# Kernel tuning notes

Measured on AMD Instinct MI355X. Metric: run time of the kernel, lower is better.

Reference implementation:

```python
import jax, jax.numpy as jnp
import numpy as np

N_EMBD = 1024  # C in forward; scale uses C**-0.5

def setup_inputs() -> dict:
    key = jax.random.key(0)
    k1, k2, k3, k4 = jax.random.split(key, 4)
    B, T, C, H = 4, 4096, N_EMBD, 64
    x = jax.random.normal(k1, (B, T, C), dtype=jnp.float32)
    # nn.Linear weights stored already-transposed as [in, out] for x @ W
    s = 1.0 / np.sqrt(C)
    Wq = jax.random.normal(k2, (C, H), dtype=jnp.float32) * s
    Wk = jax.random.normal(k3, (C, H), dtype=jnp.float32) * s
    Wv = jax.random.normal(k4, (C, H), dtype=jnp.float32) * s
    return {"x": x, "Wq": Wq, "Wk": Wk, "Wv": Wv}

def reference(x, Wq, Wk, Wv):
    B, T, C = x.shape
    q = jnp.einsum('btc,ch->bth', x, Wq)
    k = jnp.einsum('btc,ch->bth', x, Wk)
    v = jnp.einsum('btc,ch->bth', x, Wv)
    # scores scaled by C**-0.5 (note: original scales by embed dim, not head_size)
    wei = jnp.einsum('bth,bsh->bts', q, k) * (C ** -0.5)
    causal = jnp.tril(jnp.ones((T, T), dtype=bool))  # [T,T]
    wei = jnp.where(causal[None, :, :], wei, -jnp.inf)
    wei = jax.nn.softmax(wei, axis=-1)
    # dropout p=0.0 (eval-mode reference): identity
    out = jnp.einsum('bts,bsh->bth', wei, v)
    return out
```

## Files before the change

### kernel.cpp

```cpp
#include <hip/hip_runtime.h>

typedef __bf16 bf16x8 __attribute__((ext_vector_type(8)));
typedef float floatx16 __attribute__((ext_vector_type(16)));
typedef float floatx4 __attribute__((ext_vector_type(4)));

#define T_ 4096
#define STK 72
#define NSPB 144

#define WT_OFF 0u
#define Q_OFF  393216u
#define K_OFF  2490368u
#define V_OFF  4587520u
#define OP_OFF 6684672u
#define ML_OFF 25559040u

__device__ __forceinline__ unsigned short bf16bits(float f) {
  __bf16 h = (__bf16)f;
  return __builtin_bit_cast(unsigned short, h);
}

__global__ void wprep(const float* __restrict__ Wq, const float* __restrict__ Wk,
                      const float* __restrict__ Wv, __bf16* __restrict__ Wtg) {
  int idx = blockIdx.x * 256 + threadIdx.x;
  int mat = idx >> 16;
  int r = idx & 65535;
  int h = r & 63;
  int k = r >> 6;
  const float* W = (mat == 0) ? Wq : ((mat == 1) ? Wk : Wv);
  float v = W[k * 64 + h];
  if (mat == 0) v *= 0.03125f * 1.4426950408889634f;
  Wtg[(size_t)(mat * 64 + h) * 1024 + k] = (__bf16)v;
}

__global__ __launch_bounds__(256, 4) void proj(const float* __restrict__ x,
                                               const __bf16* __restrict__ Wtg,
                                               __bf16* __restrict__ Qp,
                                               __bf16* __restrict__ Kp,
                                               __bf16* __restrict__ Vp) {
  __shared__ __align__(16) unsigned short sm[(32 + 192) * STK];
  unsigned short* xt = sm;
  unsigned short* wt = sm + 32 * STK;
  const int tid = threadIdx.x;
  const int wave = tid >> 6, lane = tid & 63;
  const int wm = wave & 1, wn = wave >> 1;
  const int l15 = lane & 15, quad = lane >> 4;
  const size_t row0 = (size_t)blockIdx.x * 32;

  floatx4 acc[6];
#pragma unroll
  for (int t = 0; t < 6; t++)
#pragma unroll
    for (int i = 0; i < 4; i++) acc[t][i] = 0.0f;

  for (int kc = 0; kc < 16; ++kc) {
    __syncthreads();
    {
      int row = tid >> 3, seg = tid & 7;
      const float* src = x + (row0 + row) * 1024 + kc * 64 + seg * 8;
      float f[8];
      *(float4*)(f) = *(const float4*)(src);
      *(float4*)(f + 4) = *(const float4*)(src + 4);
      unsigned short hb[8];
#pragma unroll
      for (int i = 0; i < 8; i++) hb[i] = bf16bits(f[i]);
      *(uint4*)&xt[row * STK + seg * 8] = *(uint4*)(hb);
    }
#pragma unroll
    for (int i = 0; i < 6; i++) {
      int idx = tid + 256 * i;
      int r = idx >> 3, c = (idx & 7) * 8;
      *(uint4*)&wt[r * STK + c] = *(const uint4*)(Wtg + (size_t)r * 1024 + kc * 64 + c);
    }
    __syncthreads();
#pragma unroll
    for (int ks = 0; ks < 2; ++ks) {
      bf16x8 a = *(const bf16x8*)&xt[(wm * 16 + l15) * STK + ks * 32 + quad * 8];
#pragma unroll
      for (int ht = 0; ht < 6; ++ht) {
        bf16x8 b = *(const bf16x8*)&wt[(wn * 96 + ht * 16 + l15) * STK + ks * 32 + quad * 8];
        acc[ht] = __builtin_amdgcn_mfma_f32_16x16x32_bf16(a, b, acc[ht], 0, 0, 0);
      }
    }
  }
#pragma unroll
  for (int ht = 0; ht < 6; ++ht) {
    int g0 = wn * 96 + ht * 16;
    int mat = g0 >> 6, h0 = g0 & 63;
    __bf16* outp = (mat == 0) ? Qp : ((mat == 1) ? Kp : Vp);
#pragma unroll
    for (int r = 0; r < 4; r++) {
      size_t row = row0 + wm * 16 + quad * 4 + r;
      outp[row * 64 + h0 + l15] = (__bf16)acc[ht][r];
    }
  }
}

__global__ __launch_bounds__(256, 3) void attn1(const __bf16* __restrict__ Qp,
                                                const __bf16* __restrict__ Kp,
                                                const __bf16* __restrict__ Vp,
                                                float* __restrict__ Opart,
                                                float* __restrict__ mlpart) {
  __shared__ __align__(16) unsigned char smraw[36864];
  unsigned short* Kl = (unsigned short*)smraw;
  unsigned short* Vtl = Kl + 64 * STK;
  unsigned short* Pl = Vtl + 64 * STK;
  float* Oe = (float*)smraw;

  const int tid = threadIdx.x;
  const int wave = tid >> 6, lane = tid & 63;
  const int l31 = lane & 31, half = lane >> 5;

  const int bid = blockIdx.x;
  const int b = bid / NSPB;
  const int f = bid - b * NSPB;
  int qt = 0, cum = 0;
  for (;;) { int s = (qt + 4) >> 2; if (f < cum + s) break; cum += s; qt++; }
  const int si = f - cum;
  const int S = (qt + 4) >> 2;
  const int n_iters = 2 * (qt + 1);
  const int bbase = n_iters / S, rem = n_iters % S;
  const int it0 = si * bbase + (si < rem ? si : rem);
  const int it1 = it0 + bbase + (si < rem ? 1 : 0);

  const int qb = qt * 128;
  const size_t brow = (size_t)b * 4096;

  bf16x8 qf[4];
  {
    const __bf16* qptr = Qp + (brow + qb + wave * 32 + l31) * 64 + half * 8;
#pragma unroll
    for (int ks = 0; ks < 4; ks++) qf[ks] = *(const bf16x8*)(qptr + ks * 16);
  }

  floatx16 o0, o1;
#pragma unroll
  for (int r = 0; r < 16; r++) { o0[r] = 0.0f; o1[r] = 0.0f; }
  float m_run = -1e30f, l_run = 0.0f;
  unsigned short* Pw = Pl + wave * 32 * STK;
  const int qrow = qb + wave * 32 + l31;

  for (int it = it0; it < it1; ++it) {
    const int k0 = it * 64;
#pragma unroll
    for (int i = 0; i < 2; i++) {
      int u = tid + 256 * i;
      int kr = u >> 3, c = (u & 7) * 8;
      *(uint4*)&Kl[kr * STK + c] = *(const uint4*)(Kp + (brow + k0 + kr) * 64 + c);
    }
    {
      int kp = tid & 31, h0 = ((tid >> 5) & 7) * 8;
      const __bf16* vp = Vp + (brow + k0 + 2 * kp) * 64 + h0;
      unsigned short va[8], vb[8];
      *(uint4*)va = *(const uint4*)(vp);
      *(uint4*)vb = *(const uint4*)(vp + 64);
#pragma unroll
      for (int j = 0; j < 8; j++) {
        unsigned int w = (unsigned int)va[j] | ((unsigned int)vb[j] << 16);
        *(unsigned int*)&Vtl[(h0 + j) * STK + 2 * kp] = w;
      }
    }
    __syncthreads();
    floatx16 s0, s1;
#pragma unroll
    for (int r = 0; r < 16; r++) { s0[r] = 0.0f; s1[r] = 0.0f; }
#pragma unroll
    for (int ks = 0; ks < 4; ks++) {
      bf16x8 ka = *(const bf16x8*)&Kl[l31 * STK + ks * 16 + half * 8];
      bf16x8 kb = *(const bf16x8*)&Kl[(32 + l31) * STK + ks * 16 + half * 8];
      s0 = __builtin_amdgcn_mfma_f32_32x32x16_bf16(ka, qf[ks], s0, 0, 0, 0);
      s1 = __builtin_amdgcn_mfma_f32_32x32x16_bf16(kb, qf[ks], s1, 0, 0, 0);
    }
    if (k0 + 64 > qb) {
#pragma unroll
      for (int r = 0; r < 16; r++) {
        int rs = (r & 3) + 8 * (r >> 2) + 4 * half;
        if (k0 + rs > qrow) s0[r] = -1e30f;
        if (k0 + 32 + rs > qrow) s1[r] = -1e30f;
      }
    }
    float pm = -1e30f;
#pragma unroll
    for (int r = 0; r < 16; r++) { pm = fmaxf(pm, s0[r]); pm = fmaxf(pm, s1[r]); }
    pm = fmaxf(pm, __shfl_xor(pm, 32));
    float m_new = fmaxf(m_run, pm);
    float alpha = __builtin_amdgcn_exp2f(m_run - m_new);
    float psum = 0.0f;
#pragma unroll
    for (int r = 0; r < 16; r++) {
      s0[r] = __builtin_amdgcn_exp2f(s0[r] - m_new);
      s1[r] = __builtin_amdgcn_exp2f(s1[r] - m_new);
      psum += s0[r] + s1[r];
    }
    psum += __shfl_xor(psum, 32);
    l_run = l_run * alpha + psum;
    m_run = m_new;
#pragma unroll
    for (int r = 0; r < 16; r++) { o0[r] *= alpha; o1[r] *= alpha; }
#pragma unroll
    for (int g = 0; g < 4; ++g) {
      int kb0 = 8 * g + 4 * half;
      unsigned int w0 = (unsigned int)bf16bits(s0[4 * g]) | ((unsigned int)bf16bits(s0[4 * g + 1]) << 16);
      unsigned int w1 = (unsigned int)bf16bits(s0[4 * g + 2]) | ((unsigned int)bf16bits(s0[4 * g + 3]) << 16);
      *(uint2*)&Pw[l31 * STK + kb0] = make_uint2(w0, w1);
      unsigned int w2 = (unsigned int)bf16bits(s1[4 * g]) | ((unsigned int)bf16bits(s1[4 * g + 1]) << 16);
      unsigned int w3 = (unsigned int)bf16bits(s1[4 * g + 2]) | ((unsigned int)bf16bits(s1[4 * g + 3]) << 16);
      *(uint2*)&Pw[l31 * STK + 32 + kb0] = make_uint2(w2, w3);
    }
#pragma unroll
    for (int kst = 0; kst < 4; ++kst) {
      bf16x8 pf = *(const bf16x8*)&Pw[l31 * STK + kst * 16 + half * 8];
      bf16x8 va = *(const bf16x8*)&Vtl[l31 * STK + kst * 16 + half * 8];
      bf16x8 vb = *(const bf16x8*)&Vtl[(32 + l31) * STK + kst * 16 + half * 8];
      o0 = __builtin_amdgcn_mfma_f32_32x32x16_bf16(va, pf, o0, 0, 0, 0);
      o1 = __builtin_amdgcn_mfma_f32_32x32x16_bf16(vb, pf, o1, 0, 0, 0);
    }
    __syncthreads();
  }
#pragma unroll
  for (int r = 0; r < 16; r++) {
    int rs = (r & 3) + 8 * (r >> 2) + 4 * half;
    Oe[(wave * 32 + l31) * 68 + rs] = o0[r];
    Oe[(wave * 32 + l31) * 68 + 32 + rs] = o1[r];
  }
  if (lane < 32) {
    mlpart[(size_t)bid * 256 + wave * 32 + l31] = m_run;
    mlpart[(size_t)bid * 256 + 128 + wave * 32 + l31] = l_run;
  }
  __syncthreads();
  {
    float* dst = Opart + (size_t)bid * 8192;
    int r = tid >> 1, hh = (tid & 1) * 32;
#pragma unroll
    for (int i = 0; i < 8; i++)
      *(float4*)&dst[r * 64 + hh + 4 * i] = *(float4*)&Oe[r * 68 + hh + 4 * i];
  }
}

__global__ __launch_bounds__(256, 4) void attn2(const float* __restrict__ Opart,
                                                const float* __restrict__ mlpart,
                                                float* __restrict__ out) {
  const int bid = blockIdx.x;
  const int b = bid >> 7, rg = bid & 127;
  const int qt = rg >> 2;
  int cum = 0;
  for (int i = 0; i < qt; i++) cum += (i + 4) >> 2;
  const int S = (qt + 4) >> 2;
  const int t = threadIdx.x;
  const int r = t >> 3;
  const int prow = (rg & 3) * 32 + r;
  const int h0 = (t & 7) * 8;

  float M = -1e30f;
  for (int s = 0; s < S; s++)
    M = fmaxf(M, mlpart[(size_t)(b * NSPB + cum + s) * 256 + prow]);
  float a[8];
#pragma unroll
  for (int i = 0; i < 8; i++) a[i] = 0.0f;
  float L = 0.0f;
  for (int s = 0; s < S; s++) {
    size_t pb = (size_t)(b * NSPB + cum + s);
    float w = __builtin_amdgcn_exp2f(mlpart[pb * 256 + prow] - M);
    L += w * mlpart[pb * 256 + 128 + prow];
    const float* op = Opart + pb * 8192 + prow * 64 + h0;
    float4 v0 = *(const float4*)op;
    float4 v1 = *(const float4*)(op + 4);
    a[0] += w * v0.x; a[1] += w * v0.y; a[2] += w * v0.z; a[3] += w * v0.w;
    a[4] += w * v1.x; a[5] += w * v1.y; a[6] += w * v1.z; a[7] += w * v1.w;
  }
  float inv = 1.0f / L;
  float* po = out + ((size_t)b * 4096 + rg * 32 + r) * 64 + h0;
  float4 r0, r1;
  r0.x = a[0] * inv; r0.y = a[1] * inv; r0.z = a[2] * inv; r0.w = a[3] * inv;
  r1.x = a[4] * inv; r1.y = a[5] * inv; r1.z = a[6] * inv; r1.w = a[7] * inv;
  *(float4*)po = r0;
  *(float4*)(po + 4) = r1;
}

extern "C" void kernel_launch(void* const* d_in, const int* in_sizes, int n_in,
                              void* d_out, int out_size, void* d_ws, size_t ws_size,
                              hipStream_t stream) {
  (void)in_sizes; (void)n_in; (void)out_size; (void)ws_size;
  const float* x = (const float*)d_in[0];
  const float* Wq = (const float*)d_in[1];
  const float* Wk = (const float*)d_in[2];
  const float* Wv = (const float*)d_in[3];
  char* ws = (char*)d_ws;
  __bf16* Wtg = (__bf16*)(ws + WT_OFF);
  __bf16* Qp = (__bf16*)(ws + Q_OFF);
  __bf16* Kp = (__bf16*)(ws + K_OFF);
  __bf16* Vp = (__bf16*)(ws + V_OFF);
  float* Opart = (float*)(ws + OP_OFF);
  float* mlp = (float*)(ws + ML_OFF);
  float* out = (float*)d_out;

  hipLaunchKernelGGL(wprep, dim3(768), dim3(256), 0, stream, Wq, Wk, Wv, Wtg);
  hipLaunchKernelGGL(proj, dim3(512), dim3(256), 0, stream, x, Wtg, Qp, Kp, Vp);
  hipLaunchKernelGGL(attn1, dim3(4 * NSPB), dim3(256), 0, stream, Qp, Kp, Vp, Opart, mlp);
  hipLaunchKernelGGL(attn2, dim3(512), dim3(256), 0, stream, Opart, mlp, out);
}
```

Measured before the change: 148.9 us.

## Double attention split-K partitions and drop LDS staging in projection

The causal attention split factor changes from ceil((qt+1)/4) to ceil((qt+1)/2) splits per query tile, raising blocks per batch from 144 to 272 to improve load balance and occupancy. Partial-output buffers grow to match, and the combine kernel has to merge more partials. Separately, the projection kernel drops shared-memory staging and barriers. Each wave now loads x and W fragments directly from global memory into MFMA operands, with launch bounds relaxed to 2, which may lose reuse and coalescing.

Measured after the change: 190.1 us. +27.6%, slower.

```diff
diff --git a/kernel.cpp b/kernel.cpp
--- a/kernel.cpp
+++ b/kernel.cpp
@@ -6,14 +6,14 @@
 
 #define T_ 4096
 #define STK 72
-#define NSPB 144
+#define NSPB 272
 
 #define WT_OFF 0u
 #define Q_OFF  393216u
 #define K_OFF  2490368u
 #define V_OFF  4587520u
 #define OP_OFF 6684672u
-#define ML_OFF 25559040u
+#define ML_OFF 42336256u
 
 __device__ __forceinline__ unsigned short bf16bits(float f) {
   __bf16 h = (__bf16)f;
@@ -33,19 +33,20 @@
   Wtg[(size_t)(mat * 64 + h) * 1024 + k] = (__bf16)v;
 }
 
-__global__ __launch_bounds__(256, 4) void proj(const float* __restrict__ x,
+__global__ __launch_bounds__(256, 2) void proj(const float* __restrict__ x,
                                                const __bf16* __restrict__ Wtg,
                                                __bf16* __restrict__ Qp,
                                                __bf16* __restrict__ Kp,
                                                __bf16* __restrict__ Vp) {
-  __shared__ __align__(16) unsigned short sm[(32 + 192) * STK];
-  unsigned short* xt = sm;
-  unsigned short* wt = sm + 32 * STK;
   const int tid = threadIdx.x;
   const int wave = tid >> 6, lane = tid & 63;
-  const int wm = wave & 1, wn = wave >> 1;
   const int l15 = lane & 15, quad = lane >> 4;
-  const size_t row0 = (size_t)blockIdx.x * 32;
+  const int gw = blockIdx.x * 4 + wave;
+  const size_t row0 = (size_t)(gw >> 1) * 16;
+  const int col0 = (gw & 1) * 96;
+
+  const float* xrow = x + (row0 + l15) * 1024 + quad * 8;
+  const __bf16* wrow = Wtg + ((size_t)col0 + l15) * 1024 + quad * 8;
 
   floatx4 acc[6];
 #pragma unroll
@@ -53,44 +54,27 @@
 #pragma unroll
     for (int i = 0; i < 4; i++) acc[t][i] = 0.0f;
 
-  for (int kc = 0; kc < 16; ++kc) {
-    __syncthreads();
-    {
-      int row = tid >> 3, seg = tid & 7;
-      const float* src = x + (row0 + row) * 1024 + kc * 64 + seg * 8;
-      float f[8];
-      *(float4*)(f) = *(const float4*)(src);
-      *(float4*)(f + 4) = *(const float4*)(src + 4);
-      unsigned short hb[8];
-#pragma unroll
-      for (int i = 0; i < 8; i++) hb[i] = bf16bits(f[i]);
-      *(uint4*)&xt[row * STK + seg * 8] = *(uint4*)(hb);
-    }
-#pragma unroll
-    for (int i = 0; i < 6; i++) {
-      int idx = tid + 256 * i;
-      int r = idx >> 3, c = (idx & 7) * 8;
-      *(uint4*)&wt[r * STK + c] = *(const uint4*)(Wtg + (size_t)r * 1024 + kc * 64 + c);
-    }
-    __syncthreads();
-#pragma unroll
-    for (int ks = 0; ks < 2; ++ks) {
-      bf16x8 a = *(const bf16x8*)&xt[(wm * 16 + l15) * STK + ks * 32 + quad * 8];
-#pragma unroll
-      for (int ht = 0; ht < 6; ++ht) {
-        bf16x8 b = *(const bf16x8*)&wt[(wn * 96 + ht * 16 + l15) * STK + ks * 32 + quad * 8];
-        acc[ht] = __builtin_amdgcn_mfma_f32_16x16x32_bf16(a, b, acc[ht], 0, 0, 0);
-      }
+#pragma unroll 4
+  for (int kc = 0; kc < 32; ++kc) {
+    float4 a0 = *(const float4*)(xrow + kc * 32);
+    float4 a1 = *(const float4*)(xrow + kc * 32 + 4);
+    bf16x8 a;
+    a[0] = (__bf16)a0.x; a[1] = (__bf16)a0.y; a[2] = (__bf16)a0.z; a[3] = (__bf16)a0.w;
+    a[4] = (__bf16)a1.x; a[5] = (__bf16)a1.y; a[6] = (__bf16)a1.z; a[7] = (__bf16)a1.w;
+#pragma unroll
+    for (int ht = 0; ht < 6; ++ht) {
+      bf16x8 b = *(const bf16x8*)(wrow + (size_t)ht * 16384 + kc * 32);
+      acc[ht] = __builtin_amdgcn_mfma_f32_16x16x32_bf16(a, b, acc[ht], 0, 0, 0);
     }
   }
 #pragma unroll
   for (int ht = 0; ht < 6; ++ht) {
-    int g0 = wn * 96 + ht * 16;
+    int g0 = col0 + ht * 16;
     int mat = g0 >> 6, h0 = g0 & 63;
     __bf16* outp = (mat == 0) ? Qp : ((mat == 1) ? Kp : Vp);
 #pragma unroll
     for (int r = 0; r < 4; r++) {
-      size_t row = row0 + wm * 16 + quad * 4 + r;
+      size_t row = row0 + quad * 4 + r;
       outp[row * 64 + h0 + l15] = (__bf16)acc[ht][r];
     }
   }
@@ -115,9 +99,9 @@
   const int b = bid / NSPB;
   const int f = bid - b * NSPB;
   int qt = 0, cum = 0;
-  for (;;) { int s = (qt + 4) >> 2; if (f < cum + s) break; cum += s; qt++; }
+  for (;;) { int s = (qt + 2) >> 1; if (f < cum + s) break; cum += s; qt++; }
   const int si = f - cum;
-  const int S = (qt + 4) >> 2;
+  const int S = (qt + 2) >> 1;
   const int n_iters = 2 * (qt + 1);
   const int bbase = n_iters / S, rem = n_iters % S;
   const int it0 = si * bbase + (si < rem ? si : rem);
@@ -244,8 +228,8 @@
   const int b = bid >> 7, rg = bid & 127;
   const int qt = rg >> 2;
   int cum = 0;
-  for (int i = 0; i < qt; i++) cum += (i + 4) >> 2;
-  const int S = (qt + 4) >> 2;
+  for (int i = 0; i < qt; i++) cum += (i + 2) >> 1;
+  const int S = (qt + 2) >> 1;
   const int t = threadIdx.x;
   const int r = t >> 3;
   const int prow = (rg & 3) * 32 + r;
```

## Double-buffer projection loads via async global-to-LDS and double attention KV splits

Applied to the files above, without the earlier changes.

The projection kernel now double-buffers the x and weight tiles. Weights are loaded with global_load_lds async copies into an XOR-swizzled LDS layout, so loads for the next k-chunk overlap the MFMA work on the current one, and occupancy is lowered to 2 blocks. Separately, the attention split-K partitioning changes from ceil((qt+1)/4) to ceil((qt+1)/2) splits per query tile. That gives 272 blocks per batch and more parallelism, at the cost of more partial outputs and more combine work in attn2.

Result: slower. 154.2 us (+3.6%).

```diff
diff --git a/kernel.cpp b/kernel.cpp
--- a/kernel.cpp
+++ b/kernel.cpp
@@ -6,18 +6,23 @@
 
 #define T_ 4096
 #define STK 72
-#define NSPB 144
+#define NSPB 272
 
 #define WT_OFF 0u
 #define Q_OFF  393216u
 #define K_OFF  2490368u
 #define V_OFF  4587520u
 #define OP_OFF 6684672u
-#define ML_OFF 25559040u
+#define ML_OFF 42336256u
 
 __device__ __forceinline__ unsigned short bf16bits(float f) {
   __bf16 h = (__bf16)f;
   return __builtin_bit_cast(unsigned short, h);
+}
+
+__device__ __forceinline__ void async16(const void* g, void* l) {
+  __builtin_amdgcn_global_load_lds((const __attribute__((address_space(1))) void*)g,
+                                   (__attribute__((address_space(3))) void*)l, 16, 0, 0);
 }
 
 __global__ void wprep(const float* __restrict__ Wq, const float* __restrict__ Wk,
@@ -33,55 +38,84 @@
   Wtg[(size_t)(mat * 64 + h) * 1024 + k] = (__bf16)v;
 }
 
-__global__ __launch_bounds__(256, 4) void proj(const float* __restrict__ x,
+__global__ __launch_bounds__(256, 2) void proj(const float* __restrict__ x,
                                                const __bf16* __restrict__ Wtg,
                                                __bf16* __restrict__ Qp,
                                                __bf16* __restrict__ Kp,
                                                __bf16* __restrict__ Vp) {
-  __shared__ __align__(16) unsigned short sm[(32 + 192) * STK];
+  __shared__ __align__(16) unsigned short sm[2 * 2304 + 2 * 12288];
   unsigned short* xt = sm;
-  unsigned short* wt = sm + 32 * STK;
+  unsigned short* wt = sm + 2 * 2304;
+
   const int tid = threadIdx.x;
   const int wave = tid >> 6, lane = tid & 63;
   const int wm = wave & 1, wn = wave >> 1;
   const int l15 = lane & 15, quad = lane >> 4;
   const size_t row0 = (size_t)blockIdx.x * 32;
 
+  const int xrow = tid >> 3, xc8 = (tid & 7) * 8;
+  const float* xsrc = x + (row0 + xrow) * 1024 + xc8;
+  const int wr = tid >> 3;
+  const int wsl = tid & 7;
+
   floatx4 acc[6];
 #pragma unroll
   for (int t = 0; t < 6; t++)
 #pragma unroll
     for (int i = 0; i < 4; i++) acc[t][i] = 0.0f;
 
+  {
+    unsigned short* wb = wt;
+#pragma unroll
+    for (int i = 0; i < 6; i++) {
+      int r = wr + i * 32;
+      int sg = wsl ^ (r & 7);
+      async16((const char*)Wtg + (size_t)r * 2048 + sg * 16,
+              (char*)(wb + (i * 256 + wave * 64) * 8));
+    }
+    float f[8];
+    *(float4*)(f) = *(const float4*)(xsrc);
+    *(float4*)(f + 4) = *(const float4*)(xsrc + 4);
+    unsigned short hb[8];
+#pragma unroll
+    for (int i = 0; i < 8; i++) hb[i] = bf16bits(f[i]);
+    *(uint4*)&xt[xrow * STK + xc8] = *(uint4*)(hb);
+  }
+  __syncthreads();
+
   for (int kc = 0; kc < 16; ++kc) {
-    __syncthreads();
-    {
-      int row = tid >> 3, seg = tid & 7;
-      const float* src = x + (row0 + row) * 1024 + kc * 64 + seg * 8;
+    const int cur = kc & 1;
+    if (kc < 15) {
+      unsigned short* wb = wt + (cur ^ 1) * 12288;
+#pragma unroll
+      for (int i = 0; i < 6; i++) {
+        int r = wr + i * 32;
+        int sg = wsl ^ (r & 7);
+        async16((const char*)Wtg + (size_t)r * 2048 + (kc + 1) * 128 + sg * 16,
+                (char*)(wb + (i * 256 + wave * 64) * 8));
+      }
       float f[8];
-      *(float4*)(f) = *(const float4*)(src);
-      *(float4*)(f + 4) = *(const float4*)(src + 4);
+      *(float4*)(f) = *(const float4*)(xsrc + (kc + 1) * 64);
+      *(float4*)(f + 4) = *(const float4*)(xsrc + (kc + 1) * 64 + 4);
       unsigned short hb[8];
 #pragma unroll
       for (int i = 0; i < 8; i++) hb[i] = bf16bits(f[i]);
-      *(uint4*)&xt[row * STK + seg * 8] = *(uint4*)(hb);
-    }
-#pragma unroll
-    for (int i = 0; i < 6; i++) {
-      int idx = tid + 256 * i;
-      int r = idx >> 3, c = (idx & 7) * 8;
-      *(uint4*)&wt[r * STK + c] = *(const uint4*)(Wtg + (size_t)r * 1024 + kc * 64 + c);
-    }
-    __syncthreads();
+      *(uint4*)&xt[(cur ^ 1) * 2304 + xrow * STK + xc8] = *(uint4*)(hb);
+    }
+    const unsigned short* xb = xt + cur * 2304;
+    const unsigned short* wb = wt + cur * 12288;
 #pragma unroll
     for (int ks = 0; ks < 2; ++ks) {
-      bf16x8 a = *(const bf16x8*)&xt[(wm * 16 + l15) * STK + ks * 32 + quad * 8];
+      bf16x8 a = *(const bf16x8*)&xb[(wm * 16 + l15) * STK + ks * 32 + quad * 8];
+      int sl = (ks * 4 + quad) ^ (l15 & 7);
+      const unsigned short* wbase = wb + (wn * 96 + l15) * 64 + sl * 8;
 #pragma unroll
       for (int ht = 0; ht < 6; ++ht) {
-        bf16x8 b = *(const bf16x8*)&wt[(wn * 96 + ht * 16 + l15) * STK + ks * 32 + quad * 8];
+        bf16x8 b = *(const bf16x8*)(wbase + ht * 1024);
         acc[ht] = __builtin_amdgcn_mfma_f32_16x16x32_bf16(a, b, acc[ht], 0, 0, 0);
       }
     }
+    __syncthreads();
   }
 #pragma unroll
   for (int ht = 0; ht < 6; ++ht) {
@@ -115,9 +149,9 @@
   const int b = bid / NSPB;
   const int f = bid - b * NSPB;
   int qt = 0, cum = 0;
-  for (;;) { int s = (qt + 4) >> 2; if (f < cum + s) break; cum += s; qt++; }
+  for (;;) { int s = (qt + 2) >> 1; if (f < cum + s) break; cum += s; qt++; }
   const int si = f - cum;
-  const int S = (qt + 4) >> 2;
+  const int S = (qt + 2) >> 1;
   const int n_iters = 2 * (qt + 1);
   const int bbase = n_iters / S, rem = n_iters % S;
   const int it0 = si * bbase + (si < rem ? si : rem);
@@ -244,8 +278,8 @@
   const int b = bid >> 7, rg = bid & 127;
   const int qt = rg >> 2;
   int cum = 0;
-  for (int i = 0; i < qt; i++) cum += (i + 4) >> 2;
-  const int S = (qt + 4) >> 2;
+  for (int i = 0; i < qt; i++) cum += (i + 2) >> 1;
+  const int S = (qt + 2) >> 1;
   const int t = threadIdx.x;
   const int r = t >> 3;
   const int prow = (rg & 3) * 32 + r;
```
